# Performance work log

Measured on AMD Instinct MI355X. Metric: run time of the kernel, lower is better.

The kernel has to match this reference:

```python
import jax, jax.numpy as jnp
import numpy as np

N_EXPERTS = 8
TOP_K = 2


def setup_inputs() -> dict:
    key = jax.random.key(0)
    ks = jax.random.split(key, 5)
    B, T, D, E, H = 4, 2048, 1024, N_EXPERTS, 2730  # H = int(2*D*4/3)
    x = jax.random.normal(ks[0], (B, T, D), dtype=jnp.float32)
    gate_w = jax.random.normal(ks[1], (E, D), dtype=jnp.float32) * 0.02
    w1 = jax.random.normal(ks[2], (E, H, D), dtype=jnp.float32) * 0.02
    w3 = jax.random.normal(ks[3], (E, H, D), dtype=jnp.float32) * 0.02
    w2 = jax.random.normal(ks[4], (E, D, H), dtype=jnp.float32) * 0.02
    return {"x": x, "gate_w": gate_w, "w1": w1, "w3": w3, "w2": w2}


def reference(x, gate_w, w1, w3, w2):
    B, T, D = x.shape
    E = gate_w.shape[0]
    x_flat = x.reshape(-1, D)  # [N, D], N = B*T
    N = x_flat.shape[0]

    # Router: top-k over softmax probabilities, renormalized over selected experts
    logits = x_flat @ gate_w.T                      # [N, E]
    probs = jax.nn.softmax(logits, axis=-1)         # [N, E]
    top_v, top_i = jax.lax.top_k(probs, TOP_K)      # [N, K]
    top_v = top_v / jnp.sum(top_v, axis=-1, keepdims=True)

    # Dense combine weights [N, E]: weight of expert e for each token (0 if not selected).
    # top_k indices are distinct per token, so scatter-add equals scatter-set here.
    combine = jnp.zeros((N, E), dtype=x.dtype).at[
        jnp.arange(N)[:, None], top_i
    ].add(top_v)

    # Weighted combine of SwiGLU experts (loop over small fixed expert count).
    out = jnp.zeros_like(x_flat)
    for e in range(E):
        gate = jax.nn.silu(x_flat @ w1[e].T)        # [N, H]
        up = x_flat @ w3[e].T                       # [N, H]
        y = (gate * up) @ w2[e].T                   # [N, D]
        out = out + combine[:, e:e + 1] * y

    aux_loss = jnp.asarray(0.0, dtype=x.dtype)  # use_aux_loss=False / eval mode
    return out.reshape(B, T, D), aux_loss
```

## Files before the change

### kernel.cpp

```cpp
#include <hip/hip_runtime.h>
#include <hip/hip_bf16.h>

#define N_TOK 8192
#define D_DIM 1024
#define E_NUM 8
#define H_DIM 2730
#define HP    2816
#define NP    5632
#define NROWS (N_TOK*2)
#define MAXTILES 136
#define MAXT256  72

typedef __bf16 bf16;
typedef __bf16 bf16x8 __attribute__((ext_vector_type(8)));
typedef __bf16 bf16x4 __attribute__((ext_vector_type(4)));
typedef float  f32x4  __attribute__((ext_vector_type(4)));

__device__ __forceinline__ void gload_lds16(const bf16* g, bf16* l) {
  __builtin_amdgcn_global_load_lds((const __attribute__((address_space(1))) void*)g,
                                   (__attribute__((address_space(3))) void*)l, 16, 0, 0);
}
#define VMCNT(n) asm volatile("s_waitcnt vmcnt(" #n ")" ::: "memory")
#define LGKM0()  asm volatile("s_waitcnt lgkmcnt(0)" ::: "memory")
#define BAR() __builtin_amdgcn_s_barrier()

__global__ void conv13_kernel(const float* __restrict__ w1, const float* __restrict__ w3,
                              bf16* __restrict__ Bp) {
  int i = blockIdx.x * blockDim.x + threadIdx.x;
  if (i >= E_NUM * NP * 128) return;
  int c8 = i & 127;
  int r  = (i >> 7) % NP;
  int e  = i / (NP * 128);
  int hc = ((r >> 5) << 4) + (r & 15);
  bf16x8 o;
  if (hc < H_DIM) {
    const float* s = (((r >> 4) & 1) ? w3 : w1) + ((long)e * H_DIM + hc) * D_DIM + c8 * 8;
    float4 a0 = ((const float4*)s)[0], a1 = ((const float4*)s)[1];
    o[0]=(bf16)a0.x; o[1]=(bf16)a0.y; o[2]=(bf16)a0.z; o[3]=(bf16)a0.w;
    o[4]=(bf16)a1.x; o[5]=(bf16)a1.y; o[6]=(bf16)a1.z; o[7]=(bf16)a1.w;
  } else {
    #pragma unroll
    for (int j = 0; j < 8; j++) o[j] = (bf16)0.f;
  }
  ((bf16x8*)Bp)[i] = o;
}

__global__ void conv_w2_kernel(const float* __restrict__ src, bf16* __restrict__ dst) {
  int i = blockIdx.x * blockDim.x + threadIdx.x;
  if (i >= E_NUM * D_DIM * (HP / 8)) return;
  int c8 = i % (HP / 8);
  int row = i / (HP / 8);
  int c = c8 * 8;
  const float* s = src + (long)row * H_DIM + c;
  bf16x8 o;
  #pragma unroll
  for (int j = 0; j < 8; j++) o[j] = (c + j < H_DIM) ? (bf16)s[j] : (bf16)0.f;
  ((bf16x8*)dst)[i] = o;
}

__global__ void router_kernel(const float* __restrict__ x, const float* __restrict__ gw,
                              int* __restrict__ topi, float* __restrict__ topw,
                              int* __restrict__ counts) {
  int t = blockIdx.x * (blockDim.x >> 6) + (threadIdx.x >> 6);
  int lane = threadIdx.x & 63;
  if (t >= N_TOK) return;
  const float* xr = x + (long)t * D_DIM;
  float acc[E_NUM];
  #pragma unroll
  for (int e = 0; e < E_NUM; e++) acc[e] = 0.f;
  for (int j = 0; j < D_DIM / 64; j++) {
    float xv = xr[j * 64 + lane];
    #pragma unroll
    for (int e = 0; e < E_NUM; e++) acc[e] += xv * gw[e * D_DIM + j * 64 + lane];
  }
  #pragma unroll
  for (int e = 0; e < E_NUM; e++) {
    float v = acc[e];
    #pragma unroll
    for (int s = 32; s > 0; s >>= 1) v += __shfl_xor(v, s, 64);
    acc[e] = v;
  }
  if (lane == 0) {
    int b0 = -1, b1 = -1; float v0 = -1e30f, v1 = -1e30f;
    #pragma unroll
    for (int e = 0; e < E_NUM; e++) {
      float v = acc[e];
      if (v > v0) { v1 = v0; b1 = b0; v0 = v; b0 = e; }
      else if (v > v1) { v1 = v; b1 = e; }
    }
    float w0 = 1.f / (1.f + expf(v1 - v0));
    topi[t * 2] = b0; topi[t * 2 + 1] = b1;
    topw[t * 2] = w0; topw[t * 2 + 1] = 1.f - w0;
    atomicAdd(&counts[b0], 1); atomicAdd(&counts[b1], 1);
  }
}

__global__ void tiles_kernel(const int* __restrict__ counts, int* __restrict__ offs,
                             int* __restrict__ tlist, int* __restrict__ tlist2) {
  if (threadIdx.x == 0) {
    int s = 0, idx = 0, idx2 = 0;
    for (int e = 0; e < E_NUM; e++) {
      offs[e] = s;
      int ne = counts[e];
      s += ne;
      int nt = (ne + 127) >> 7;
      for (int t = 0; t < nt; t++) tlist[idx++] = (e << 8) | t;
      int nt2 = (ne + 255) >> 8;
      for (int t = 0; t < nt2; t++) tlist2[idx2++] = (e << 8) | t;
    }
    offs[E_NUM] = s;
    for (; idx < MAXTILES; idx++) tlist[idx] = -1;
    for (; idx2 < MAXT256; idx2++) tlist2[idx2] = -1;
  }
}

__global__ void scatter_kernel(const int* __restrict__ topi, const float* __restrict__ topw,
                               const int* __restrict__ offs, int* __restrict__ cursor,
                               int* __restrict__ rowmap, float* __restrict__ roww,
                               int* __restrict__ rowoftok) {
  int i = blockIdx.x * blockDim.x + threadIdx.x;
  if (i >= NROWS) return;
  int e = topi[i];
  int pos = atomicAdd(&cursor[e], 1);
  int row = offs[e] + pos;
  rowmap[row] = i >> 1;
  roww[row] = topw[i];
  rowoftok[i] = row;
}

__global__ void gather_kernel(const float* __restrict__ x, const int* __restrict__ rowmap,
                              bf16* __restrict__ Xg) {
  int r = blockIdx.x * (blockDim.x >> 6) + (threadIdx.x >> 6);
  int lane = threadIdx.x & 63;
  if (r >= NROWS) return;
  int t = rowmap[r];
  const float4* src = (const float4*)(x + (long)t * D_DIM);
  bf16x4* dst = (bf16x4*)(Xg + (long)r * D_DIM);
  #pragma unroll
  for (int j = 0; j < 4; j++) {
    float4 v = src[j * 64 + lane];
    bf16x4 o; o[0]=(bf16)v.x; o[1]=(bf16)v.y; o[2]=(bf16)v.z; o[3]=(bf16)v.w;
    dst[j * 64 + lane] = o;
  }
}

__global__ void combine_kernel(const bf16* __restrict__ y, const int* __restrict__ rowoftok,
                               const float* __restrict__ topw, float* __restrict__ out) {
  int t = blockIdx.x * (blockDim.x >> 6) + (threadIdx.x >> 6);
  int lane = threadIdx.x & 63;
  if (t >= N_TOK) return;
  int r0 = rowoftok[t * 2], r1 = rowoftok[t * 2 + 1];
  float w0 = topw[t * 2], w1 = topw[t * 2 + 1];
  const bf16x8* y0 = (const bf16x8*)(y + (long)r0 * D_DIM);
  const bf16x8* y1 = (const bf16x8*)(y + (long)r1 * D_DIM);
  float* o = out + (long)t * D_DIM;
  #pragma unroll
  for (int j = 0; j < 2; j++) {
    bf16x8 a = y0[j * 64 + lane], b = y1[j * 64 + lane];
    float4 v0, v1;
    v0.x = w0*(float)a[0] + w1*(float)b[0]; v0.y = w0*(float)a[1] + w1*(float)b[1];
    v0.z = w0*(float)a[2] + w1*(float)b[2]; v0.w = w0*(float)a[3] + w1*(float)b[3];
    v1.x = w0*(float)a[4] + w1*(float)b[4]; v1.y = w0*(float)a[5] + w1*(float)b[5];
    v1.z = w0*(float)a[6] + w1*(float)b[6]; v1.w = w0*(float)a[7] + w1*(float)b[7];
    float4* op = (float4*)(o + (j * 64 + lane) * 8);
    op[0] = v0; op[1] = v1;
  }
}


#define G1_STAGE(SB, T) do { \
    _Pragma("unroll") for (int L_ = 0; L_ < 4; L_++) \
      gload_lds16(aS[L_] + (T) * 32, smem + (SB) + w * 2048 + L_ * 512); \
    _Pragma("unroll") for (int L_ = 0; L_ < 2; L_++) \
      gload_lds16(bS[L_] + (T) * 32, smem + (SB) + 8192 + w * 1024 + L_ * 512); \
  } while (0)

#define G1_READ0(SB) do { \
    _Pragma("unroll") for (int m_ = 0; m_ < 4; m_++) \
      af[m_] = *(const bf16x8*)&smem[(SB) + (w * 64 + m_ * 16 + fr) * 32 + qp]; \
    _Pragma("unroll") for (int q_ = 0; q_ < 4; q_++) \
      bf0[q_] = *(const bf16x8*)&smem[(SB) + 8192 + (q_ * 16 + fr) * 32 + qp]; \
  } while (0)

#define G1_MFMA0() do { __builtin_amdgcn_s_setprio(1); \
    _Pragma("unroll") for (int m_ = 0; m_ < 4; m_++) \
    _Pragma("unroll") for (int q_ = 0; q_ < 4; q_++) \
      acc[m_][q_] = __builtin_amdgcn_mfma_f32_16x16x32_bf16(af[m_], bf0[q_], acc[m_][q_], 0, 0, 0); \
    __builtin_amdgcn_s_setprio(0); } while (0)

#define G1_READ1(SB) do { \
    _Pragma("unroll") for (int q_ = 0; q_ < 4; q_++) \
      bf1[q_] = *(const bf16x8*)&smem[(SB) + 8192 + ((q_ + 4) * 16 + fr) * 32 + qp]; \
  } while (0)

#define G1_MFMA1() do { __builtin_amdgcn_s_setprio(1); \
    _Pragma("unroll") for (int m_ = 0; m_ < 4; m_++) \
    _Pragma("unroll") for (int q_ = 0; q_ < 4; q_++) \
      acc[m_][q_ + 4] = __builtin_amdgcn_mfma_f32_16x16x32_bf16(af[m_], bf1[q_], acc[m_][q_ + 4], 0, 0, 0); \
    __builtin_amdgcn_s_setprio(0); } while (0)

__global__ __launch_bounds__(256, 2) void gemm1_kernel(
    const bf16* __restrict__ Xg, const bf16* __restrict__ Bp,
    const int* __restrict__ counts, const int* __restrict__ offs,
    const int* __restrict__ tlist2, bf16* __restrict__ h) {
  int bid = blockIdx.x;
  int tile = bid / 44, col = bid - tile * 44;
  int te = tlist2[tile];
  if (te < 0) return;
  int e = te >> 8, tm = te & 255;
  int ne = counts[e];
  int row_base = offs[e];
  int n0 = col * 128;

  __shared__ bf16 smem[3 * 12288];
  int tid = threadIdx.x, w = tid >> 6, lane = tid & 63;
  int fr = lane & 15, hi = lane >> 4;
  int qp = (hi ^ ((fr >> 1) & 3)) * 8;
  int srcq = ((lane & 3) ^ ((lane >> 3) & 3)) * 8;
  int srow = lane >> 2;

  f32x4 acc[4][8];
  #pragma unroll
  for (int m = 0; m < 4; m++)
    #pragma unroll
    for (int q = 0; q < 8; q++) acc[m][q] = (f32x4)0.f;

  const bf16* Bpe = Bp + (long)e * NP * D_DIM;
  const bf16* aS[4];
  const bf16* bS[2];
  #pragma unroll
  for (int L = 0; L < 4; L++) {
    int ra = row_base + min(tm * 256 + w * 64 + L * 16 + srow, ne - 1);
    aS[L] = Xg + (long)ra * D_DIM + srcq;
  }
  #pragma unroll
  for (int L = 0; L < 2; L++) {
    int rb = n0 + w * 32 + L * 16 + srow;
    bS[L] = Bpe + (long)rb * D_DIM + srcq;
  }

  bf16x8 af[4], bf0[4], bf1[4];

  G1_STAGE(0, 0); G1_STAGE(12288, 1);
  VMCNT(6); BAR();

  int sbC = 0, sbS = 24576;
  for (int t = 0; t < 30; t++) {
    G1_READ0(sbC);
    G1_STAGE(sbS, t + 2);
    BAR();
    G1_MFMA0();
    G1_READ1(sbC);
    G1_MFMA1();
    LGKM0(); VMCNT(6); BAR();
    sbC += 12288; if (sbC > 24576) sbC = 0;
    sbS += 12288; if (sbS > 24576) sbS = 0;
  }
  { G1_READ0(sbC); BAR(); G1_MFMA0(); G1_READ1(sbC); G1_MFMA1(); LGKM0(); VMCNT(0); BAR();
    sbC += 12288; if (sbC > 24576) sbC = 0; }
  { G1_READ0(sbC); G1_MFMA0(); G1_READ1(sbC); G1_MFMA1(); }

  int crow4 = hi * 4;
  #pragma unroll
  for (int m = 0; m < 4; m++)
    #pragma unroll
    for (int j = 0; j < 4; j++) {
      int rloc = tm * 256 + w * 64 + m * 16 + crow4 + j;
      if (rloc < ne) {
        long hrow = (long)(row_base + rloc) * HP;
        #pragma unroll
        for (int p = 0; p < 4; p++) {
          int col2 = (n0 >> 1) + p * 16 + fr;
          float g = acc[m][2 * p][j], u = acc[m][2 * p + 1][j];
          h[hrow + col2] = (bf16)((g / (1.f + __expf(-g))) * u);
        }
      }
    }
}

#define G2_STAGE(SB, T) do { \
    _Pragma("unroll") for (int L_ = 0; L_ < 2; L_++) \
      gload_lds16(aS[L_] + (T) * 32, smem2 + (SB) + w * 1024 + L_ * 512); \
    _Pragma("unroll") for (int L_ = 0; L_ < 4; L_++) \
      gload_lds16(bS[L_] + (T) * 32, smem2 + (SB) + 4096 + (L_ * 4 + w) * 512); \
  } while (0)

#define G2_READ0(SB) do { \
    _Pragma("unroll") for (int m_ = 0; m_ < 4; m_++) \
      af[m_] = *(const bf16x8*)&smem2[(SB) + (wr * 64 + m_ * 16 + fr) * 32 + qp]; \
    _Pragma("unroll") for (int n_ = 0; n_ < 4; n_++) \
      bf0[n_] = *(const bf16x8*)&smem2[(SB) + 4096 + (wc * 128 + n_ * 16 + fr) * 32 + qp]; \
  } while (0)

#define G2_MFMA0() do { __builtin_amdgcn_s_setprio(1); \
    _Pragma("unroll") for (int m_ = 0; m_ < 4; m_++) \
    _Pragma("unroll") for (int n_ = 0; n_ < 4; n_++) \
      acc[m_][n_] = __builtin_amdgcn_mfma_f32_16x16x32_bf16(af[m_], bf0[n_], acc[m_][n_], 0, 0, 0); \
    __builtin_amdgcn_s_setprio(0); } while (0)

#define G2_READ1(SB) do { \
    _Pragma("unroll") for (int n_ = 0; n_ < 4; n_++) \
      bf1[n_] = *(const bf16x8*)&smem2[(SB) + 4096 + (wc * 128 + (n_ + 4) * 16 + fr) * 32 + qp]; \
  } while (0)

#define G2_MFMA1() do { __builtin_amdgcn_s_setprio(1); \
    _Pragma("unroll") for (int m_ = 0; m_ < 4; m_++) \
    _Pragma("unroll") for (int n_ = 0; n_ < 4; n_++) \
      acc[m_][n_ + 4] = __builtin_amdgcn_mfma_f32_16x16x32_bf16(af[m_], bf1[n_], acc[m_][n_ + 4], 0, 0, 0); \
    __builtin_amdgcn_s_setprio(0); } while (0)

__global__ __launch_bounds__(256, 2) void gemm2_kernel(
    const bf16* __restrict__ h, const bf16* __restrict__ w2b,
    const int* __restrict__ counts, const int* __restrict__ offs,
    const int* __restrict__ tlist, bf16* __restrict__ y) {
  int bid = blockIdx.x;
  int tile = bid >> 2, col = bid & 3;
  int te = tlist[tile];
  if (te < 0) return;
  int e = te >> 8, tm = te & 255;
  int ne = counts[e];
  int row_base = offs[e];
  int n0 = col * 256;

  __shared__ bf16 smem2[3 * 12288];
  int tid = threadIdx.x, w = tid >> 6, lane = tid & 63;
  int wr = w >> 1, wc = w & 1;
  int fr = lane & 15, hi = lane >> 4;
  int qp = (hi ^ ((fr >> 1) & 3)) * 8;
  int srcq = ((lane & 3) ^ ((lane >> 3) & 3)) * 8;
  int srow = lane >> 2;

  f32x4 acc[4][8];
  #pragma unroll
  for (int m = 0; m < 4; m++)
    #pragma unroll
    for (int n = 0; n < 8; n++) acc[m][n] = (f32x4)0.f;

  const bf16* w2e = w2b + (long)e * D_DIM * HP;
  const bf16* aS[2];
  const bf16* bS[4];
  #pragma unroll
  for (int L = 0; L < 2; L++) {
    int ra = row_base + min(tm * 128 + w * 32 + L * 16 + srow, ne - 1);
    aS[L] = h + (long)ra * HP + srcq;
  }
  #pragma unroll
  for (int L = 0; L < 4; L++) {
    int rb = n0 + (L * 4 + w) * 16 + srow;
    bS[L] = w2e + (long)rb * HP + srcq;
  }

  bf16x8 af[4], bf0[4], bf1[4];

  G2_STAGE(0, 0); G2_STAGE(12288, 1);
  VMCNT(6); BAR();

  int sbC = 0, sbS = 24576;
  for (int t = 0; t < 86; t++) {
    G2_READ0(sbC);
    G2_STAGE(sbS, t + 2);
    BAR();
    G2_MFMA0();
    G2_READ1(sbC);
    G2_MFMA1();
    LGKM0(); VMCNT(6); BAR();
    sbC += 12288; if (sbC > 24576) sbC = 0;
    sbS += 12288; if (sbS > 24576) sbS = 0;
  }
  { G2_READ0(sbC); BAR(); G2_MFMA0(); G2_READ1(sbC); G2_MFMA1(); LGKM0(); VMCNT(0); BAR();
    sbC += 12288; if (sbC > 24576) sbC = 0; }
  { G2_READ0(sbC); G2_MFMA0(); G2_READ1(sbC); G2_MFMA1(); }

  int crow4 = hi * 4;
  #pragma unroll
  for (int m = 0; m < 4; m++)
    #pragma unroll
    for (int j = 0; j < 4; j++) {
      int rloc = tm * 128 + wr * 64 + m * 16 + crow4 + j;
      if (rloc < ne) {
        long yrow = (long)(row_base + rloc) * D_DIM;
        #pragma unroll
        for (int n = 0; n < 8; n++) {
          int col2 = n0 + wc * 128 + n * 16 + fr;
          y[yrow + col2] = (bf16)acc[m][n][j];
        }
      }
    }
}

extern "C" void kernel_launch(void* const* d_in, const int* in_sizes, int n_in,
                              void* d_out, int out_size, void* d_ws, size_t ws_size,
                              hipStream_t stream) {
  const float* x  = (const float*)d_in[0];
  const float* gw = (const float*)d_in[1];
  const float* w1 = (const float*)d_in[2];
  const float* w3 = (const float*)d_in[3];
  const float* w2 = (const float*)d_in[4];
  float* out = (float*)d_out;

  char* ws = (char*)d_ws;
  int*   counts   = (int*)(ws);
  int*   cursor   = (int*)(ws + 64);
  int*   offs     = (int*)(ws + 128);
  int*   tlist    = (int*)(ws + 192);
  int*   tlist2   = (int*)(ws + 768);
  int*   topi     = (int*)(ws + 2048);
  float* topw     = (float*)(ws + 2048 + 65536);
  int*   rowmap   = (int*)(ws + 2048 + 131072);
  float* roww     = (float*)(ws + 2048 + 196608);
  int*   rowoftok = (int*)(ws + 2048 + 262144);
  char*  big      = ws + 2048 + 327680;
  bf16* Bp   = (bf16*)big;
  bf16* w2b  = (bf16*)big;
  bf16* Xg   = Bp + (size_t)E_NUM * NP * D_DIM;
  bf16* hbuf = Xg + (size_t)NROWS * D_DIM;
  bf16* ybuf = Xg;

  hipMemsetAsync((char*)d_out + (size_t)(out_size - 1) * sizeof(float), 0, sizeof(float), stream);
  hipMemsetAsync(ws, 0, 256, stream);

  int nbp = E_NUM * NP * 128;
  conv13_kernel<<<(nbp + 255) / 256, 256, 0, stream>>>(w1, w3, Bp);

  router_kernel<<<N_TOK / 4, 256, 0, stream>>>(x, gw, topi, topw, counts);
  tiles_kernel<<<1, 64, 0, stream>>>(counts, offs, tlist, tlist2);
  scatter_kernel<<<(NROWS + 255) / 256, 256, 0, stream>>>(topi, topw, offs, cursor, rowmap, roww, rowoftok);
  gather_kernel<<<NROWS / 4, 256, 0, stream>>>(x, rowmap, Xg);

  gemm1_kernel<<<MAXT256 * 44, 256, 0, stream>>>(Xg, Bp, counts, offs, tlist2, hbuf);

  int w2n = E_NUM * D_DIM * (HP / 8);
  conv_w2_kernel<<<(w2n + 255) / 256, 256, 0, stream>>>(w2, w2b);

  gemm2_kernel<<<MAXTILES * 4, 256, 0, stream>>>(hbuf, w2b, counts, offs, tlist, ybuf);
  combine_kernel<<<N_TOK / 4, 256, 0, stream>>>(ybuf, rowoftok, topw, out);
}
```

Baseline: 724.6 us.

## Retile gemm2 to 256x128 tiles reusing the 256-row tile list

Changes the second grouped GEMM from 128-row by 256-column tiles to 256-row by 128-column tiles, so each wave owns 64 rows across the full 128 columns. The kernel now reuses the 256-row tile list already built for gemm1, and the separate 128-row list is removed. This changes the A/B staging split in LDS (more activation rows, fewer weight rows per stage) and the grid shape. The aim is for each loaded weight column block to be reused across more tokens. The cost is coarser row padding for experts whose token counts don't fill a 256-row tile.

```diff
diff --git a/kernel.cpp b/kernel.cpp
--- a/kernel.cpp
+++ b/kernel.cpp
@@ -8,7 +8,6 @@
 #define HP    2816
 #define NP    5632
 #define NROWS (N_TOK*2)
-#define MAXTILES 136
 #define MAXT256  72
 
 typedef __bf16 bf16;
@@ -96,20 +95,17 @@
 }
 
 __global__ void tiles_kernel(const int* __restrict__ counts, int* __restrict__ offs,
-                             int* __restrict__ tlist, int* __restrict__ tlist2) {
+                             int* __restrict__ tlist2) {
   if (threadIdx.x == 0) {
-    int s = 0, idx = 0, idx2 = 0;
+    int s = 0, idx2 = 0;
     for (int e = 0; e < E_NUM; e++) {
       offs[e] = s;
       int ne = counts[e];
       s += ne;
-      int nt = (ne + 127) >> 7;
-      for (int t = 0; t < nt; t++) tlist[idx++] = (e << 8) | t;
       int nt2 = (ne + 255) >> 8;
       for (int t = 0; t < nt2; t++) tlist2[idx2++] = (e << 8) | t;
     }
     offs[E_NUM] = s;
-    for (; idx < MAXTILES; idx++) tlist[idx] = -1;
     for (; idx2 < MAXT256; idx2++) tlist2[idx2] = -1;
   }
 }
@@ -279,52 +275,51 @@
 }
 
 #define G2_STAGE(SB, T) do { \
+    _Pragma("unroll") for (int L_ = 0; L_ < 4; L_++) \
+      gload_lds16(aS[L_] + (T) * 32, smem2 + (SB) + w * 2048 + L_ * 512); \
     _Pragma("unroll") for (int L_ = 0; L_ < 2; L_++) \
-      gload_lds16(aS[L_] + (T) * 32, smem2 + (SB) + w * 1024 + L_ * 512); \
-    _Pragma("unroll") for (int L_ = 0; L_ < 4; L_++) \
-      gload_lds16(bS[L_] + (T) * 32, smem2 + (SB) + 4096 + (L_ * 4 + w) * 512); \
+      gload_lds16(bS[L_] + (T) * 32, smem2 + (SB) + 8192 + w * 1024 + L_ * 512); \
   } while (0)
 
 #define G2_READ0(SB) do { \
     _Pragma("unroll") for (int m_ = 0; m_ < 4; m_++) \
-      af[m_] = *(const bf16x8*)&smem2[(SB) + (wr * 64 + m_ * 16 + fr) * 32 + qp]; \
-    _Pragma("unroll") for (int n_ = 0; n_ < 4; n_++) \
-      bf0[n_] = *(const bf16x8*)&smem2[(SB) + 4096 + (wc * 128 + n_ * 16 + fr) * 32 + qp]; \
+      af[m_] = *(const bf16x8*)&smem2[(SB) + (w * 64 + m_ * 16 + fr) * 32 + qp]; \
+    _Pragma("unroll") for (int q_ = 0; q_ < 4; q_++) \
+      bf0[q_] = *(const bf16x8*)&smem2[(SB) + 8192 + (q_ * 16 + fr) * 32 + qp]; \
   } while (0)
 
 #define G2_MFMA0() do { __builtin_amdgcn_s_setprio(1); \
     _Pragma("unroll") for (int m_ = 0; m_ < 4; m_++) \
-    _Pragma("unroll") for (int n_ = 0; n_ < 4; n_++) \
-      acc[m_][n_] = __builtin_amdgcn_mfma_f32_16x16x32_bf16(af[m_], bf0[n_], acc[m_][n_], 0, 0, 0); \
+    _Pragma("unroll") for (int q_ = 0; q_ < 4; q_++) \
+      acc[m_][q_] = __builtin_amdgcn_mfma_f32_16x16x32_bf16(af[m_], bf0[q_], acc[m_][q_], 0, 0, 0); \
     __builtin_amdgcn_s_setprio(0); } while (0)
 
 #define G2_READ1(SB) do { \
-    _Pragma("unroll") for (int n_ = 0; n_ < 4; n_++) \
-      bf1[n_] = *(const bf16x8*)&smem2[(SB) + 4096 + (wc * 128 + (n_ + 4) * 16 + fr) * 32 + qp]; \
+    _Pragma("unroll") for (int q_ = 0; q_ < 4; q_++) \
+      bf1[q_] = *(const bf16x8*)&smem2[(SB) + 8192 + ((q_ + 4) * 16 + fr) * 32 + qp]; \
   } while (0)
 
 #define G2_MFMA1() do { __builtin_amdgcn_s_setprio(1); \
     _Pragma("unroll") for (int m_ = 0; m_ < 4; m_++) \
-    _Pragma("unroll") for (int n_ = 0; n_ < 4; n_++) \
-      acc[m_][n_ + 4] = __builtin_amdgcn_mfma_f32_16x16x32_bf16(af[m_], bf1[n_], acc[m_][n_ + 4], 0, 0, 0); \
+    _Pragma("unroll") for (int q_ = 0; q_ < 4; q_++) \
+      acc[m_][q_ + 4] = __builtin_amdgcn_mfma_f32_16x16x32_bf16(af[m_], bf1[q_], acc[m_][q_ + 4], 0, 0, 0); \
     __builtin_amdgcn_s_setprio(0); } while (0)
 
 __global__ __launch_bounds__(256, 2) void gemm2_kernel(
     const bf16* __restrict__ h, const bf16* __restrict__ w2b,
     const int* __restrict__ counts, const int* __restrict__ offs,
-    const int* __restrict__ tlist, bf16* __restrict__ y) {
+    const int* __restrict__ tlist2, bf16* __restrict__ y) {
   int bid = blockIdx.x;
-  int tile = bid >> 2, col = bid & 3;
-  int te = tlist[tile];
+  int tile = bid >> 3, col = bid & 7;
+  int te = tlist2[tile];
   if (te < 0) return;
   int e = te >> 8, tm = te & 255;
   int ne = counts[e];
   int row_base = offs[e];
-  int n0 = col * 256;
+  int n0 = col * 128;
 
   __shared__ bf16 smem2[3 * 12288];
   int tid = threadIdx.x, w = tid >> 6, lane = tid & 63;
-  int wr = w >> 1, wc = w & 1;
   int fr = lane & 15, hi = lane >> 4;
   int qp = (hi ^ ((fr >> 1) & 3)) * 8;
   int srcq = ((lane & 3) ^ ((lane >> 3) & 3)) * 8;
@@ -334,19 +329,19 @@
   #pragma unroll
   for (int m = 0; m < 4; m++)
     #pragma unroll
-    for (int n = 0; n < 8; n++) acc[m][n] = (f32x4)0.f;
+    for (int q = 0; q < 8; q++) acc[m][q] = (f32x4)0.f;
 
   const bf16* w2e = w2b + (long)e * D_DIM * HP;
-  const bf16* aS[2];
-  const bf16* bS[4];
+  const bf16* aS[4];
+  const bf16* bS[2];
+  #pragma unroll
+  for (int L = 0; L < 4; L++) {
+    int ra = row_base + min(tm * 256 + w * 64 + L * 16 + srow, ne - 1);
+    aS[L] = h + (long)ra * HP + srcq;
+  }
   #pragma unroll
   for (int L = 0; L < 2; L++) {
-    int ra = row_base + min(tm * 128 + w * 32 + L * 16 + srow, ne - 1);
-    aS[L] = h + (long)ra * HP + srcq;
-  }
-  #pragma unroll
-  for (int L = 0; L < 4; L++) {
-    int rb = n0 + (L * 4 + w) * 16 + srow;
+    int rb = n0 + w * 32 + L * 16 + srow;
     bS[L] = w2e + (long)rb * HP + srcq;
   }
 
@@ -376,13 +371,13 @@
   for (int m = 0; m < 4; m++)
     #pragma unroll
     for (int j = 0; j < 4; j++) {
-      int rloc = tm * 128 + wr * 64 + m * 16 + crow4 + j;
+      int rloc = tm * 256 + w * 64 + m * 16 + crow4 + j;
       if (rloc < ne) {
         long yrow = (long)(row_base + rloc) * D_DIM;
         #pragma unroll
-        for (int n = 0; n < 8; n++) {
-          int col2 = n0 + wc * 128 + n * 16 + fr;
-          y[yrow + col2] = (bf16)acc[m][n][j];
+        for (int q = 0; q < 8; q++) {
+          int col2 = n0 + q * 16 + fr;
+          y[yrow + col2] = (bf16)acc[m][q][j];
         }
       }
     }
@@ -402,7 +397,6 @@
   int*   counts   = (int*)(ws);
   int*   cursor   = (int*)(ws + 64);
   int*   offs     = (int*)(ws + 128);
-  int*   tlist    = (int*)(ws + 192);
   int*   tlist2   = (int*)(ws + 768);
   int*   topi     = (int*)(ws + 2048);
   float* topw     = (float*)(ws + 2048 + 65536);
@@ -423,7 +417,7 @@
   conv13_kernel<<<(nbp + 255) / 256, 256, 0, stream>>>(w1, w3, Bp);
 
   router_kernel<<<N_TOK / 4, 256, 0, stream>>>(x, gw, topi, topw, counts);
-  tiles_kernel<<<1, 64, 0, stream>>>(counts, offs, tlist, tlist2);
+  tiles_kernel<<<1, 64, 0, stream>>>(counts, offs, tlist2);
   scatter_kernel<<<(NROWS + 255) / 256, 256, 0, stream>>>(topi, topw, offs, cursor, rowmap, roww, rowoftok);
   gather_kernel<<<NROWS / 4, 256, 0, stream>>>(x, rowmap, Xg);
 
@@ -432,6 +426,6 @@
   int w2n = E_NUM * D_DIM * (HP / 8);
   conv_w2_kernel<<<(w2n + 255) / 256, 256, 0, stream>>>(w2, w2b);
 
-  gemm2_kernel<<<MAXTILES * 4, 256, 0, stream>>>(hbuf, w2b, counts, offs, tlist, ybuf);
+  gemm2_kernel<<<MAXT256 * 8, 256, 0, stream>>>(hbuf, w2b, counts, offs, tlist2, ybuf);
   combine_kernel<<<N_TOK / 4, 256, 0, stream>>>(ybuf, rowoftok, topw, out);
 }
```

Result: slower. 741.7 us (+2.4%).
